# Kernel tuning notes

Measured on AMD Instinct MI355X. Metric: run time of the kernel, lower is better.

## Reference

```python
import jax, jax.numpy as jnp
import numpy as np

N_NODES = 50000
N_EDGES = 800000
IN_F, HID, HEADS, OUT_F = 64, 64, 4, 64
NEG_SLOPE = 0.2


def _gat_conv(x, ei, W, a_src, a_dst, b, H, C):
    """PyG-style GATConv (eval mode, add_self_loops=True, concat=True).
    x: [N, F_in], ei: [2, E], W: [F_in, H*C], a_src/a_dst: [H, C], b: [H*C].
    """
    N = x.shape[0]
    h = (x @ W).reshape(N, H, C)                      # [N,H,C]
    asrc = jnp.einsum('nhc,hc->nh', h, a_src)         # [N,H]
    adst = jnp.einsum('nhc,hc->nh', h, a_dst)         # [N,H]
    src, dst = ei[0], ei[1]
    logits = jax.nn.leaky_relu(asrc[src] + adst[dst], NEG_SLOPE)  # [E,H]
    m = jax.ops.segment_max(logits, dst, num_segments=N)
    m = jnp.where(jnp.isfinite(m), m, 0.0)
    ex = jnp.exp(logits - m[dst])
    denom = jax.ops.segment_sum(ex, dst, num_segments=N)
    alpha = ex / (denom[dst] + 1e-16)                 # [E,H]
    msg = h[src] * alpha[:, :, None]                  # [E,H,C]
    out = jax.ops.segment_sum(msg, dst, num_segments=N)  # [N,H,C]
    return out.reshape(N, H * C) + b


def _add_self_loops(ei, n):
    loops = jnp.arange(n, dtype=ei.dtype)
    return jnp.concatenate([ei, jnp.stack([loops, loops])], axis=1)


def setup_inputs() -> dict:
    key = jax.random.key(0)
    ks = jax.random.split(key, 16)
    x = jax.random.normal(ks[0], (N_NODES, IN_F), dtype=jnp.float32)
    edge_index = jax.random.randint(ks[1], (2, N_EDGES), 0, N_NODES, dtype=jnp.int32)
    s = 0.1
    d = {'x': x, 'edge_index': edge_index}
    # layer 0: IN_F -> HID, HEADS heads
    d['W0'] = jax.random.normal(ks[2], (IN_F, HEADS * HID), jnp.float32) * s
    d['a_src0'] = jax.random.normal(ks[3], (HEADS, HID), jnp.float32) * s
    d['a_dst0'] = jax.random.normal(ks[4], (HEADS, HID), jnp.float32) * s
    d['b0'] = jnp.zeros((HEADS * HID,), jnp.float32)
    # layer 1: HEADS*HID -> HID, HEADS heads
    d['W1'] = jax.random.normal(ks[5], (HEADS * HID, HEADS * HID), jnp.float32) * s
    d['a_src1'] = jax.random.normal(ks[6], (HEADS, HID), jnp.float32) * s
    d['a_dst1'] = jax.random.normal(ks[7], (HEADS, HID), jnp.float32) * s
    d['b1'] = jnp.zeros((HEADS * HID,), jnp.float32)
    # layer 2: HEADS*HID -> OUT_F, 1 head
    d['W2'] = jax.random.normal(ks[8], (HEADS * HID, OUT_F), jnp.float32) * s
    d['a_src2'] = jax.random.normal(ks[9], (1, OUT_F), jnp.float32) * s
    d['a_dst2'] = jax.random.normal(ks[10], (1, OUT_F), jnp.float32) * s
    d['b2'] = jnp.zeros((OUT_F,), jnp.float32)
    return d


def reference(x, edge_index, W0, a_src0, a_dst0, b0, W1, a_src1, a_dst1, b1, W2, a_src2, a_dst2, b2):
    ei = _add_self_loops(edge_index, x.shape[0])
    h = _gat_conv(x, ei, W0, a_src0, a_dst0, b0, HEADS, HID)
    h = jax.nn.elu(h)  # dropout identity in eval
    h = _gat_conv(h, ei, W1, a_src1, a_dst1, b1, HEADS, HID)
    h = jax.nn.elu(h)
    out = _gat_conv(h, ei, W2, a_src2, a_dst2, b2, 1, OUT_F)
    return out
```

## Files before the change

### kernel.cpp

```cpp
#include <hip/hip_runtime.h>
#include <hip/hip_fp16.h>
#include <math.h>

#define NODES 50000
#define EDGES 800000
#define NB_SCAN ((NODES + 1023) / 1024)

typedef __attribute__((ext_vector_type(8))) _Float16 f16x8;
typedef __attribute__((ext_vector_type(4))) _Float16 f16x4;
typedef __attribute__((ext_vector_type(4))) float f32x4;

__device__ __forceinline__ float lrelu02(float x){ return x > 0.f ? x : 0.2f * x; }


__global__ __launch_bounds__(256) void gat_zero(int* __restrict__ p, int n){
  int i = blockIdx.x * 256 + threadIdx.x;
  if (i < n) p[i] = 0;
}

__global__ __launch_bounds__(256) void gat_hist(const int* __restrict__ ei, int* __restrict__ cnt){
  int e = blockIdx.x * 256 + threadIdx.x;
  if (e < EDGES) atomicAdd(&cnt[ei[EDGES + e]], 1);
}

__global__ __launch_bounds__(256) void gat_blocksum(const int* __restrict__ cnt, int* __restrict__ bsums){
  __shared__ int sd[256];
  int t = threadIdx.x, b = blockIdx.x;
  int base = b * 1024 + t * 4, s = 0;
  #pragma unroll
  for (int j = 0; j < 4; j++){ int i = base + j; if (i < NODES) s += cnt[i]; }
  sd[t] = s; __syncthreads();
  for (int o = 128; o > 0; o >>= 1){ if (t < o) sd[t] += sd[t + o]; __syncthreads(); }
  if (t == 0) bsums[b] = sd[0];
}

__global__ void gat_scan_bsums(int* bsums, int nb){
  if (threadIdx.x == 0 && blockIdx.x == 0){
    int run = 0;
    for (int i = 0; i < nb; i++){ int v = bsums[i]; bsums[i] = run; run += v; }
  }
}

__global__ __launch_bounds__(256) void gat_rowptr(int* __restrict__ cnt, const int* __restrict__ bsums,
                                                  int* __restrict__ row_ptr){
  __shared__ int sd[256];
  int t = threadIdx.x, b = blockIdx.x;
  int base = b * 1024 + t * 4;
  int c[4]; int s = 0;
  #pragma unroll
  for (int j = 0; j < 4; j++){
    int i = base + j;
    c[j] = (i < NODES) ? cnt[i] : 0;
    s += c[j];
    if (i < NODES) cnt[i] = 0;
  }
  sd[t] = s; __syncthreads();
  for (int o = 1; o < 256; o <<= 1){
    int v = (t >= o) ? sd[t - o] : 0;
    __syncthreads();
    if (t >= o) sd[t] += v;
    __syncthreads();
  }
  int off = bsums[b] + sd[t] - s;
  #pragma unroll
  for (int j = 0; j < 4; j++){
    int i = base + j;
    if (i < NODES){ row_ptr[i] = off; off += c[j]; }
  }
  if (b == 0 && t == 0) row_ptr[NODES] = EDGES;
}

__global__ __launch_bounds__(256) void gat_scatter(const int* __restrict__ ei, const int* __restrict__ row_ptr,
                                                    int* __restrict__ fill, int* __restrict__ col,
                                                    int* __restrict__ dstarr){
  int e = blockIdx.x * 256 + threadIdx.x;
  if (e < EDGES){
    int s = ei[e], d = ei[EDGES + e];
    int pos = row_ptr[d] + atomicAdd(&fill[d], 1);
    col[pos] = s;
    dstarr[pos] = d;
  }
}


__global__ __launch_bounds__(256) void gat_cvt_h(const float* __restrict__ src, _Float16* __restrict__ dst, int n4){
  int i = blockIdx.x * 256 + threadIdx.x;
  if (i < n4){
    float4 v = *(const float4*)(src + (size_t)i * 4);
    f16x4 h = { (_Float16)v.x, (_Float16)v.y, (_Float16)v.z, (_Float16)v.w };
    *(f16x4*)(dst + (size_t)i * 4) = h;
  }
}

__global__ __launch_bounds__(256) void gat_wt(const float* __restrict__ W, _Float16* __restrict__ Wt, int K, int N){
  int n = blockIdx.x * 256 + threadIdx.x;
  int k = blockIdx.y;
  if (n < N) Wt[(size_t)n * K + k] = (_Float16)W[(size_t)k * N + n];
}

__global__ __launch_bounds__(256) void gat_ws0(const float* __restrict__ W0, const float* __restrict__ a_src0,
                                               const float* __restrict__ a_dst0,
                                               float* __restrict__ ws, float* __restrict__ wd){
  int t = threadIdx.x;
  int h = t >> 6, c = t & 63;
  float s = 0.f, d = 0.f;
  for (int cc = 0; cc < 64; cc++){
    float w = W0[(size_t)c * 256 + h * 64 + cc];
    s += w * a_src0[h * 64 + cc];
    d += w * a_dst0[h * 64 + cc];
  }
  ws[h * 64 + c] = s;
  wd[h * 64 + c] = d;
}


template<int K, int N>
__global__ __launch_bounds__(256) void gat_gemm_mfma(const _Float16* __restrict__ A, const _Float16* __restrict__ Wt,
                                                      _Float16* __restrict__ C, int M){
  constexpr int NT = N / 64;
  constexpr int LDT = 40;
  __shared__ _Float16 As[64][LDT];
  __shared__ _Float16 Bs[N][LDT];

  int tid = threadIdx.x;
  int w = tid >> 6, l = tid & 63;
  int lg = l >> 4, lr = l & 15;
  int bm = blockIdx.x * 64;

  f32x4 acc[4][NT];
  #pragma unroll
  for (int m = 0; m < 4; m++)
    #pragma unroll
    for (int n = 0; n < NT; n++)
      acc[m][n] = (f32x4){0.f, 0.f, 0.f, 0.f};

  int ar = tid >> 2;
  int akc = (tid & 3) * 8;
  bool avalid = (bm + ar) < M;
  const _Float16* aptr = A + (size_t)(bm + ar) * K + akc;

  for (int k0 = 0; k0 < K; k0 += 32){
    float4 av = avalid ? *(const float4*)(aptr + k0) : make_float4(0.f, 0.f, 0.f, 0.f);
    __syncthreads();
    *(float4*)&As[ar][akc] = av;
    #pragma unroll
    for (int c = 0; c < N / 64; c++){
      int idx = c * 256 + tid;
      int n = idx >> 2, kc = (idx & 3) * 8;
      *(float4*)&Bs[n][kc] = *(const float4*)(Wt + (size_t)n * K + k0 + kc);
    }
    __syncthreads();

    f16x8 af[4], bf[NT];
    #pragma unroll
    for (int m = 0; m < 4; m++) af[m] = *(const f16x8*)&As[16 * m + lr][8 * lg];
    #pragma unroll
    for (int n = 0; n < NT; n++) bf[n] = *(const f16x8*)&Bs[w * (N / 4) + 16 * n + lr][8 * lg];
    #pragma unroll
    for (int m = 0; m < 4; m++)
      #pragma unroll
      for (int n = 0; n < NT; n++)
        acc[m][n] = __builtin_amdgcn_mfma_f32_16x16x32_f16(af[m], bf[n], acc[m][n], 0, 0, 0);
  }

  #pragma unroll
  for (int m = 0; m < 4; m++){
    #pragma unroll
    for (int j = 0; j < 4; j++){
      int row = bm + 16 * m + 4 * lg + j;
      if (row < M){
        #pragma unroll
        for (int n = 0; n < NT; n++)
          C[(size_t)row * N + w * (N / 4) + 16 * n + lr] = (_Float16)acc[m][n][j];
      }
    }
  }
}


__global__ __launch_bounds__(256) void gat_gemm_bd(const _Float16* __restrict__ A, const _Float16* __restrict__ Bt,
                                                    const float* __restrict__ bias, _Float16* __restrict__ C, int M){
  int tid = threadIdx.x;
  int w = tid >> 6, l = tid & 63;
  int lg = l >> 4, lr = l & 15;
  int bm = blockIdx.x * 64;

  f32x4 acc[4][4];
  #pragma unroll
  for (int m = 0; m < 4; m++)
    #pragma unroll
    for (int n = 0; n < 4; n++)
      acc[m][n] = (f32x4){0.f, 0.f, 0.f, 0.f};

  f16x8 zf = {};
  #pragma unroll
  for (int ks = 0; ks < 2; ks++){
    int koff = ks * 32;
    f16x8 af[4], bf[4];
    #pragma unroll
    for (int m = 0; m < 4; m++){
      int row = bm + 16 * m + lr;
      af[m] = (row < M) ? *(const f16x8*)(A + (size_t)row * 256 + w * 64 + koff + 8 * lg) : zf;
    }
    #pragma unroll
    for (int n = 0; n < 4; n++)
      bf[n] = *(const f16x8*)(Bt + (size_t)(w * 64 + 16 * n + lr) * 64 + koff + 8 * lg);
    #pragma unroll
    for (int m = 0; m < 4; m++)
      #pragma unroll
      for (int n = 0; n < 4; n++)
        acc[m][n] = __builtin_amdgcn_mfma_f32_16x16x32_f16(af[m], bf[n], acc[m][n], 0, 0, 0);
  }

  #pragma unroll
  for (int m = 0; m < 4; m++){
    #pragma unroll
    for (int j = 0; j < 4; j++){
      int row = bm + 16 * m + 4 * lg + j;
      if (row < M){
        #pragma unroll
        for (int n = 0; n < 4; n++){
          int cc = w * 64 + 16 * n + lr;
          float o = acc[m][n][j] + bias[cc];
          o = o > 0.f ? o : expm1f(o);
          C[(size_t)row * 256 + cc] = (_Float16)o;
        }
      }
    }
  }
}


__global__ __launch_bounds__(256) void gat_attn0(const _Float16* __restrict__ xh, const float* __restrict__ ws,
                                                  const float* __restrict__ wd,
                                                  float* __restrict__ asrc, float* __restrict__ adst, int N){
  int lane = threadIdx.x & 63;
  int wid = threadIdx.x >> 6;
  int n = blockIdx.x * 4 + wid;
  if (n >= N) return;
  float v = (float)xh[(size_t)n * 64 + lane];
  #pragma unroll
  for (int h = 0; h < 4; h++){
    float s1 = v * ws[h * 64 + lane];
    float s2 = v * wd[h * 64 + lane];
    #pragma unroll
    for (int o = 32; o > 0; o >>= 1){ s1 += __shfl_xor(s1, o); s2 += __shfl_xor(s2, o); }
    if (lane == 0){ asrc[n * 4 + h] = s1; adst[n * 4 + h] = s2; }
  }
}

__global__ __launch_bounds__(256) void gat_attn4(const _Float16* __restrict__ h, const float* __restrict__ a_src,
                                                  const float* __restrict__ a_dst,
                                                  float* __restrict__ asrc, float* __restrict__ adst, int N){
  int lane = threadIdx.x & 63;
  int wid = threadIdx.x >> 6;
  int n = blockIdx.x * 4 + wid;
  if (n >= N) return;
  int co = lane * 4;
  f16x4 hv = *(const f16x4*)(h + (size_t)n * 256 + co);
  float4 av = *(const float4*)&a_src[co];
  float4 dv = *(const float4*)&a_dst[co];
  float f0 = (float)hv[0], f1 = (float)hv[1], f2 = (float)hv[2], f3 = (float)hv[3];
  float s1 = f0 * av.x + f1 * av.y + f2 * av.z + f3 * av.w;
  float s2 = f0 * dv.x + f1 * dv.y + f2 * dv.z + f3 * dv.w;
  #pragma unroll
  for (int o = 8; o > 0; o >>= 1){ s1 += __shfl_xor(s1, o); s2 += __shfl_xor(s2, o); }
  if ((lane & 15) == 0){
    int q = lane >> 4;
    asrc[n * 4 + q] = s1;
    adst[n * 4 + q] = s2;
  }
}

__global__ __launch_bounds__(256) void gat_attn1(const _Float16* __restrict__ h, const float* __restrict__ a_src,
                                                  const float* __restrict__ a_dst,
                                                  float* __restrict__ asrc, float* __restrict__ adst, int N){
  int lane = threadIdx.x & 63;
  int wid = threadIdx.x >> 6;
  int n = blockIdx.x * 4 + wid;
  if (n >= N) return;
  float v = (float)h[(size_t)n * 64 + lane];
  float s1 = v * a_src[lane];
  float s2 = v * a_dst[lane];
  #pragma unroll
  for (int o = 32; o > 0; o >>= 1){ s1 += __shfl_xor(s1, o); s2 += __shfl_xor(s2, o); }
  if (lane == 0){ asrc[n] = s1; adst[n] = s2; }
}


__global__ __launch_bounds__(256) void gat_edge_exp0(const int* __restrict__ col, const int* __restrict__ dstarr,
                                                      const float* __restrict__ asrc, const float* __restrict__ adst,
                                                      float* __restrict__ exf){
  int i = blockIdx.x * 256 + threadIdx.x;
  if (i >= EDGES) return;
  int s = col[i], d = dstarr[i];
  float4 a = *(const float4*)&asrc[s * 4];
  float4 b = *(const float4*)&adst[d * 4];
  float4 r;
  r.x = __expf(lrelu02(a.x + b.x));
  r.y = __expf(lrelu02(a.y + b.y));
  r.z = __expf(lrelu02(a.z + b.z));
  r.w = __expf(lrelu02(a.w + b.w));
  *(float4*)&exf[(size_t)i * 4] = r;
}


__global__ __launch_bounds__(256) void gat_aggregate_in64(const _Float16* __restrict__ xh, const float* __restrict__ exf,
                                                           const float* __restrict__ asrc, const float* __restrict__ adst,
                                                           const int* __restrict__ row_ptr, const int* __restrict__ col,
                                                           _Float16* __restrict__ agg){
  int lane = threadIdx.x & 63;
  int wid = threadIdx.x >> 6;
  int d = blockIdx.x * 4 + wid;
  if (d >= NODES) return;

  float4 ad4 = *(const float4*)&adst[d * 4];
  float4 a4  = *(const float4*)&asrc[d * 4];
  float ex0 = __expf(lrelu02(a4.x + ad4.x));
  float ex1 = __expf(lrelu02(a4.y + ad4.y));
  float ex2 = __expf(lrelu02(a4.z + ad4.z));
  float ex3 = __expf(lrelu02(a4.w + ad4.w));
  float xv = (float)xh[(size_t)d * 64 + lane];
  float acc0 = ex0 * xv, acc1 = ex1 * xv, acc2 = ex2 * xv, acc3 = ex3 * xv;
  float den0 = ex0, den1 = ex1, den2 = ex2, den3 = ex3;

  int e0 = row_ptr[d], e1 = row_ptr[d + 1];
  const _Float16* xbase = xh + lane;
  int e = e0;
  for (; e + 4 <= e1; e += 4){
    int s0 = col[e], s1 = col[e + 1], s2 = col[e + 2], s3 = col[e + 3];
    float4 fA = *(const float4*)(exf + (size_t)(e)     * 4);
    float4 fB = *(const float4*)(exf + (size_t)(e + 1) * 4);
    float4 fC = *(const float4*)(exf + (size_t)(e + 2) * 4);
    float4 fD = *(const float4*)(exf + (size_t)(e + 3) * 4);
    float v0 = (float)xbase[(size_t)s0 * 64];
    float v1 = (float)xbase[(size_t)s1 * 64];
    float v2 = (float)xbase[(size_t)s2 * 64];
    float v3 = (float)xbase[(size_t)s3 * 64];
    den0 += fA.x + fB.x + fC.x + fD.x;
    den1 += fA.y + fB.y + fC.y + fD.y;
    den2 += fA.z + fB.z + fC.z + fD.z;
    den3 += fA.w + fB.w + fC.w + fD.w;
    acc0 += fA.x * v0 + fB.x * v1 + fC.x * v2 + fD.x * v3;
    acc1 += fA.y * v0 + fB.y * v1 + fC.y * v2 + fD.y * v3;
    acc2 += fA.z * v0 + fB.z * v1 + fC.z * v2 + fD.z * v3;
    acc3 += fA.w * v0 + fB.w * v1 + fC.w * v2 + fD.w * v3;
  }
  for (; e < e1; e++){
    int s0 = col[e];
    float4 fA = *(const float4*)(exf + (size_t)e * 4);
    float v0 = (float)xbase[(size_t)s0 * 64];
    den0 += fA.x; den1 += fA.y; den2 += fA.z; den3 += fA.w;
    acc0 += fA.x * v0; acc1 += fA.y * v0; acc2 += fA.z * v0; acc3 += fA.w * v0;
  }

  _Float16* ob = agg + (size_t)d * 256 + lane;
  ob[0]   = (_Float16)(acc0 / (den0 + 1e-16f));
  ob[64]  = (_Float16)(acc1 / (den1 + 1e-16f));
  ob[128] = (_Float16)(acc2 / (den2 + 1e-16f));
  ob[192] = (_Float16)(acc3 / (den3 + 1e-16f));
}


template<bool DOELU>
__global__ __launch_bounds__(256) void gat_aggregate4(const _Float16* __restrict__ hH, const float* __restrict__ asrc,
                                                       const float* __restrict__ adst,
                                                       const int* __restrict__ row_ptr, const int* __restrict__ col,
                                                       const float* __restrict__ bias, _Float16* __restrict__ out){
  int lane = threadIdx.x & 63;
  int wid = threadIdx.x >> 6;
  int d = blockIdx.x * 4 + wid;
  if (d >= NODES) return;
  int q = lane >> 4;
  int co = lane * 4;

  float adq = adst[d * 4 + q];

  float ex = __expf(lrelu02(asrc[d * 4 + q] + adq));
  f16x4 hv = *(const f16x4*)(hH + (size_t)d * 256 + co);
  float4 acc = make_float4(ex * (float)hv[0], ex * (float)hv[1], ex * (float)hv[2], ex * (float)hv[3]);
  float den = ex;

  int e0 = row_ptr[d], e1 = row_ptr[d + 1];
  const _Float16* hbase = hH + co;
  int e = e0;
  for (; e + 4 <= e1; e += 4){
    int s0 = col[e], s1 = col[e + 1], s2 = col[e + 2], s3 = col[e + 3];
    float a0 = asrc[s0 * 4 + q], a1 = asrc[s1 * 4 + q], a2 = asrc[s2 * 4 + q], a3 = asrc[s3 * 4 + q];
    f16x4 h0 = *(const f16x4*)(hbase + (size_t)s0 * 256);
    f16x4 h1 = *(const f16x4*)(hbase + (size_t)s1 * 256);
    f16x4 h2 = *(const f16x4*)(hbase + (size_t)s2 * 256);
    f16x4 h3 = *(const f16x4*)(hbase + (size_t)s3 * 256);
    float x0 = __expf(lrelu02(a0 + adq));
    float x1 = __expf(lrelu02(a1 + adq));
    float x2 = __expf(lrelu02(a2 + adq));
    float x3 = __expf(lrelu02(a3 + adq));
    den += x0 + x1 + x2 + x3;
    acc.x += x0 * (float)h0[0] + x1 * (float)h1[0] + x2 * (float)h2[0] + x3 * (float)h3[0];
    acc.y += x0 * (float)h0[1] + x1 * (float)h1[1] + x2 * (float)h2[1] + x3 * (float)h3[1];
    acc.z += x0 * (float)h0[2] + x1 * (float)h1[2] + x2 * (float)h2[2] + x3 * (float)h3[2];
    acc.w += x0 * (float)h0[3] + x1 * (float)h1[3] + x2 * (float)h2[3] + x3 * (float)h3[3];
  }
  for (; e < e1; e++){
    int s0 = col[e];
    float a0 = asrc[s0 * 4 + q];
    f16x4 h0 = *(const f16x4*)(hbase + (size_t)s0 * 256);
    float x0 = __expf(lrelu02(a0 + adq));
    den += x0;
    acc.x += x0 * (float)h0[0]; acc.y += x0 * (float)h0[1];
    acc.z += x0 * (float)h0[2]; acc.w += x0 * (float)h0[3];
  }

  float inv = 1.f / (den + 1e-16f);
  float4 b4 = *(const float4*)&bias[co];
  float4 o = make_float4(acc.x * inv + b4.x, acc.y * inv + b4.y, acc.z * inv + b4.z, acc.w * inv + b4.w);
  if (DOELU){
    o.x = o.x > 0.f ? o.x : expm1f(o.x);
    o.y = o.y > 0.f ? o.y : expm1f(o.y);
    o.z = o.z > 0.f ? o.z : expm1f(o.z);
    o.w = o.w > 0.f ? o.w : expm1f(o.w);
  }
  f16x4 oh = { (_Float16)o.x, (_Float16)o.y, (_Float16)o.z, (_Float16)o.w };
  *(f16x4*)(out + (size_t)d * 256 + co) = oh;
}

__global__ __launch_bounds__(256) void gat_aggregate1(const _Float16* __restrict__ hH, const float* __restrict__ asrc,
                                                       const float* __restrict__ adst,
                                                       const int* __restrict__ row_ptr, const int* __restrict__ col,
                                                       const float* __restrict__ bias, float* __restrict__ out){
  int lane = threadIdx.x & 63;
  int wid = threadIdx.x >> 6;
  int d = blockIdx.x * 4 + wid;
  if (d >= NODES) return;

  float adq = adst[d];
  float ex = __expf(lrelu02(asrc[d] + adq));
  float acc = ex * (float)hH[(size_t)d * 64 + lane];
  float den = ex;

  int e0 = row_ptr[d], e1 = row_ptr[d + 1];
  const _Float16* hbase = hH + lane;
  int e = e0;
  for (; e + 4 <= e1; e += 4){
    int s0 = col[e], s1 = col[e + 1], s2 = col[e + 2], s3 = col[e + 3];
    float a0 = asrc[s0], a1 = asrc[s1], a2 = asrc[s2], a3 = asrc[s3];
    float v0 = (float)hbase[(size_t)s0 * 64];
    float v1 = (float)hbase[(size_t)s1 * 64];
    float v2 = (float)hbase[(size_t)s2 * 64];
    float v3 = (float)hbase[(size_t)s3 * 64];
    float x0 = __expf(lrelu02(a0 + adq));
    float x1 = __expf(lrelu02(a1 + adq));
    float x2 = __expf(lrelu02(a2 + adq));
    float x3 = __expf(lrelu02(a3 + adq));
    den += x0 + x1 + x2 + x3;
    acc += x0 * v0 + x1 * v1 + x2 * v2 + x3 * v3;
  }
  for (; e < e1; e++){
    int s0 = col[e];
    float x0 = __expf(lrelu02(asrc[s0] + adq));
    den += x0;
    acc += x0 * (float)hbase[(size_t)s0 * 64];
  }
  out[(size_t)d * 64 + lane] = acc / (den + 1e-16f) + bias[lane];
}


extern "C" void kernel_launch(void* const* d_in, const int* in_sizes, int n_in,
                              void* d_out, int out_size, void* d_ws, size_t ws_size,
                              hipStream_t stream) {
  const float* x   = (const float*)d_in[0];
  const int*   ei  = (const int*)  d_in[1];
  const float* W0  = (const float*)d_in[2];
  const float* as0 = (const float*)d_in[3];
  const float* ad0 = (const float*)d_in[4];
  const float* b0  = (const float*)d_in[5];
  const float* W1  = (const float*)d_in[6];
  const float* as1 = (const float*)d_in[7];
  const float* ad1 = (const float*)d_in[8];
  const float* b1  = (const float*)d_in[9];
  const float* W2  = (const float*)d_in[10];
  const float* as2 = (const float*)d_in[11];
  const float* ad2 = (const float*)d_in[12];
  const float* b2  = (const float*)d_in[13];
  float* out = (float*)d_out;

  auto al = [](size_t v){ return (v + 255) & ~(size_t)255; };
  char* p = (char*)d_ws;
  int*      row_ptr = (int*)p;      p += al((NODES + 1) * sizeof(int));
  int*      cnt     = (int*)p;      p += al(NODES * sizeof(int));
  int*      bsums   = (int*)p;      p += al(64 * sizeof(int));
  int*      col     = (int*)p;      p += al(EDGES * sizeof(int));
  int*      dstarr  = (int*)p;      p += al(EDGES * sizeof(int));
  float*    exf     = (float*)p;    p += al((size_t)EDGES * 4 * sizeof(float));
  float*    asrc    = (float*)p;    p += al(NODES * 4 * sizeof(float));
  float*    adst    = (float*)p;    p += al(NODES * 4 * sizeof(float));
  _Float16* xh      = (_Float16*)p; p += al((size_t)NODES * 64 * sizeof(_Float16));
  _Float16* hH      = (_Float16*)p; p += al((size_t)NODES * 256 * sizeof(_Float16));
  _Float16* actb    = (_Float16*)p; p += al((size_t)NODES * 256 * sizeof(_Float16));
  _Float16* Wt0     = (_Float16*)p; p += al(256 * 64 * sizeof(_Float16));
  _Float16* Wt1     = (_Float16*)p; p += al(256 * 256 * sizeof(_Float16));
  _Float16* Wt2     = (_Float16*)p; p += al(64 * 256 * sizeof(_Float16));
  float*    ws0     = (float*)p;    p += al(256 * sizeof(float));
  float*    wd0     = (float*)p;    p += al(256 * sizeof(float));

  gat_cvt_h<<<(NODES * 64 / 4 + 255) / 256, 256, 0, stream>>>(x, xh, NODES * 64 / 4);
  gat_wt<<<dim3(1, 64), 256, 0, stream>>>(W0, Wt0, 64, 256);
  gat_wt<<<dim3(1, 256), 256, 0, stream>>>(W1, Wt1, 256, 256);
  gat_wt<<<dim3(1, 256), 256, 0, stream>>>(W2, Wt2, 256, 64);
  gat_ws0<<<1, 256, 0, stream>>>(W0, as0, ad0, ws0, wd0);

  gat_zero<<<(NODES + 255) / 256, 256, 0, stream>>>(cnt, NODES);
  gat_hist<<<(EDGES + 255) / 256, 256, 0, stream>>>(ei, cnt);
  gat_blocksum<<<NB_SCAN, 256, 0, stream>>>(cnt, bsums);
  gat_scan_bsums<<<1, 64, 0, stream>>>(bsums, NB_SCAN);
  gat_rowptr<<<NB_SCAN, 256, 0, stream>>>(cnt, bsums, row_ptr);
  gat_scatter<<<(EDGES + 255) / 256, 256, 0, stream>>>(ei, row_ptr, cnt, col, dstarr);

  const int nodeBlocks = (NODES + 3) / 4;
  const int gemmBlocks = (NODES + 63) / 64;
  const int edgeBlocks = (EDGES + 255) / 256;

  gat_attn0<<<nodeBlocks, 256, 0, stream>>>(xh, ws0, wd0, asrc, adst, NODES);
  gat_edge_exp0<<<edgeBlocks, 256, 0, stream>>>(col, dstarr, asrc, adst, exf);
  gat_aggregate_in64<<<nodeBlocks, 256, 0, stream>>>(xh, exf, asrc, adst, row_ptr, col, hH);
  gat_gemm_bd<<<gemmBlocks, 256, 0, stream>>>(hH, Wt0, b0, actb, NODES);

  gat_gemm_mfma<256, 256><<<gemmBlocks, 256, 0, stream>>>(actb, Wt1, hH, NODES);
  gat_attn4<<<nodeBlocks, 256, 0, stream>>>(hH, as1, ad1, asrc, adst, NODES);
  gat_aggregate4<true><<<nodeBlocks, 256, 0, stream>>>(hH, asrc, adst, row_ptr, col, b1, actb);

  gat_gemm_mfma<256, 64><<<gemmBlocks, 256, 0, stream>>>(actb, Wt2, hH, NODES);
  gat_attn1<<<nodeBlocks, 256, 0, stream>>>(hH, as2, ad2, asrc, adst, NODES);
  gat_aggregate1<<<nodeBlocks, 256, 0, stream>>>(hH, asrc, adst, row_ptr, col, b2, out);
}
```

Before: 377.9 us.

## Precompute head-major edge exps and split layer-1 aggregation per head

For the middle layer, a new edge kernel computes the per-edge exponentials once and stores them head-major. The aggregation kernel then launches one block per head per group of four nodes, so each wavefront handles a single head with 64 channels and reads a contiguous stream of exps instead of recomputing exp from gathered asrc. The gather and aggregation loops in all layers also get an alignment prologue, then load column indices as int4, and the layer-1 and layer-2 loops are unrolled by 8. This trades an extra edge pass and more blocks, each re-reading row_ptr and col per head, for more memory-level parallelism and less exp work inside the aggregation.

```diff
diff --git a/kernel.cpp b/kernel.cpp
--- a/kernel.cpp
+++ b/kernel.cpp
@@ -304,6 +304,20 @@
   *(float4*)&exf[(size_t)i * 4] = r;
 }
 
+__global__ __launch_bounds__(256) void gat_edge_exp4h(const int* __restrict__ col, const int* __restrict__ dstarr,
+                                                       const float* __restrict__ asrc, const float* __restrict__ adst,
+                                                       float* __restrict__ exfh){
+  int i = blockIdx.x * 256 + threadIdx.x;
+  if (i >= EDGES) return;
+  int s = col[i], d = dstarr[i];
+  float4 a = *(const float4*)&asrc[s * 4];
+  float4 b = *(const float4*)&adst[d * 4];
+  exfh[i]             = __expf(lrelu02(a.x + b.x));
+  exfh[EDGES + i]     = __expf(lrelu02(a.y + b.y));
+  exfh[2 * EDGES + i] = __expf(lrelu02(a.z + b.z));
+  exfh[3 * EDGES + i] = __expf(lrelu02(a.w + b.w));
+}
+
 
 __global__ __launch_bounds__(256) void gat_aggregate_in64(const _Float16* __restrict__ xh, const float* __restrict__ exf,
                                                            const float* __restrict__ asrc, const float* __restrict__ adst,
@@ -327,16 +341,23 @@
   int e0 = row_ptr[d], e1 = row_ptr[d + 1];
   const _Float16* xbase = xh + lane;
   int e = e0;
+  for (; e < e1 && (e & 3); e++){
+    int s0 = col[e];
+    float4 fA = *(const float4*)(exf + (size_t)e * 4);
+    float v0 = (float)xbase[(size_t)s0 * 64];
+    den0 += fA.x; den1 += fA.y; den2 += fA.z; den3 += fA.w;
+    acc0 += fA.x * v0; acc1 += fA.y * v0; acc2 += fA.z * v0; acc3 += fA.w * v0;
+  }
   for (; e + 4 <= e1; e += 4){
-    int s0 = col[e], s1 = col[e + 1], s2 = col[e + 2], s3 = col[e + 3];
+    int4 c4 = *(const int4*)&col[e];
     float4 fA = *(const float4*)(exf + (size_t)(e)     * 4);
     float4 fB = *(const float4*)(exf + (size_t)(e + 1) * 4);
     float4 fC = *(const float4*)(exf + (size_t)(e + 2) * 4);
     float4 fD = *(const float4*)(exf + (size_t)(e + 3) * 4);
-    float v0 = (float)xbase[(size_t)s0 * 64];
-    float v1 = (float)xbase[(size_t)s1 * 64];
-    float v2 = (float)xbase[(size_t)s2 * 64];
-    float v3 = (float)xbase[(size_t)s3 * 64];
+    float v0 = (float)xbase[(size_t)c4.x * 64];
+    float v1 = (float)xbase[(size_t)c4.y * 64];
+    float v2 = (float)xbase[(size_t)c4.z * 64];
+    float v3 = (float)xbase[(size_t)c4.w * 64];
     den0 += fA.x + fB.x + fC.x + fD.x;
     den1 += fA.y + fB.y + fC.y + fD.y;
     den2 += fA.z + fB.z + fC.z + fD.z;
@@ -362,67 +383,59 @@
 }
 
 
-template<bool DOELU>
-__global__ __launch_bounds__(256) void gat_aggregate4(const _Float16* __restrict__ hH, const float* __restrict__ asrc,
-                                                       const float* __restrict__ adst,
-                                                       const int* __restrict__ row_ptr, const int* __restrict__ col,
-                                                       const float* __restrict__ bias, _Float16* __restrict__ out){
-  int lane = threadIdx.x & 63;
-  int wid = threadIdx.x >> 6;
-  int d = blockIdx.x * 4 + wid;
-  if (d >= NODES) return;
-  int q = lane >> 4;
-  int co = lane * 4;
+__global__ __launch_bounds__(256) void gat_aggregate4h(const _Float16* __restrict__ hH,
+                                                        const float* __restrict__ exfh,
+                                                        const float* __restrict__ asrc, const float* __restrict__ adst,
+                                                        const int* __restrict__ row_ptr, const int* __restrict__ col,
+                                                        const float* __restrict__ bias, _Float16* __restrict__ out){
+  int bid = blockIdx.x;
+  int r = bid & 7;
+  int q = r >> 1;
+  int dq = (bid >> 3) * 2 + (r & 1);
+  int lane = threadIdx.x & 63, w = threadIdx.x >> 6;
+  int d = dq * 4 + w;
 
   float adq = adst[d * 4 + q];
-
   float ex = __expf(lrelu02(asrc[d * 4 + q] + adq));
-  f16x4 hv = *(const f16x4*)(hH + (size_t)d * 256 + co);
-  float4 acc = make_float4(ex * (float)hv[0], ex * (float)hv[1], ex * (float)hv[2], ex * (float)hv[3]);
   float den = ex;
-
+  const _Float16* hb = hH + q * 64 + lane;
+  float acc = ex * (float)hb[(size_t)d * 256];
+
+  const float* eq = exfh + (size_t)q * EDGES;
   int e0 = row_ptr[d], e1 = row_ptr[d + 1];
-  const _Float16* hbase = hH + co;
   int e = e0;
-  for (; e + 4 <= e1; e += 4){
-    int s0 = col[e], s1 = col[e + 1], s2 = col[e + 2], s3 = col[e + 3];
-    float a0 = asrc[s0 * 4 + q], a1 = asrc[s1 * 4 + q], a2 = asrc[s2 * 4 + q], a3 = asrc[s3 * 4 + q];
-    f16x4 h0 = *(const f16x4*)(hbase + (size_t)s0 * 256);
-    f16x4 h1 = *(const f16x4*)(hbase + (size_t)s1 * 256);
-    f16x4 h2 = *(const f16x4*)(hbase + (size_t)s2 * 256);
-    f16x4 h3 = *(const f16x4*)(hbase + (size_t)s3 * 256);
-    float x0 = __expf(lrelu02(a0 + adq));
-    float x1 = __expf(lrelu02(a1 + adq));
-    float x2 = __expf(lrelu02(a2 + adq));
-    float x3 = __expf(lrelu02(a3 + adq));
-    den += x0 + x1 + x2 + x3;
-    acc.x += x0 * (float)h0[0] + x1 * (float)h1[0] + x2 * (float)h2[0] + x3 * (float)h3[0];
-    acc.y += x0 * (float)h0[1] + x1 * (float)h1[1] + x2 * (float)h2[1] + x3 * (float)h3[1];
-    acc.z += x0 * (float)h0[2] + x1 * (float)h1[2] + x2 * (float)h2[2] + x3 * (float)h3[2];
-    acc.w += x0 * (float)h0[3] + x1 * (float)h1[3] + x2 * (float)h2[3] + x3 * (float)h3[3];
+  for (; e < e1 && (e & 3); e++){
+    float ee = eq[e];
+    den += ee; acc += ee * (float)hb[(size_t)col[e] * 256];
+  }
+  for (; e + 8 <= e1; e += 8){
+    int4 cA = *(const int4*)&col[e];
+    int4 cB = *(const int4*)&col[e + 4];
+    float4 eA = *(const float4*)&eq[e];
+    float4 eB = *(const float4*)&eq[e + 4];
+    float v0 = (float)hb[(size_t)cA.x * 256];
+    float v1 = (float)hb[(size_t)cA.y * 256];
+    float v2 = (float)hb[(size_t)cA.z * 256];
+    float v3 = (float)hb[(size_t)cA.w * 256];
+    float v4 = (float)hb[(size_t)cB.x * 256];
+    float v5 = (float)hb[(size_t)cB.y * 256];
+    float v6 = (float)hb[(size_t)cB.z * 256];
+    float v7 = (float)hb[(size_t)cB.w * 256];
+    den += eA.x + eA.y + eA.z + eA.w + eB.x + eB.y + eB.z + eB.w;
+    acc += eA.x * v0 + eA.y * v1 + eA.z * v2 + eA.w * v3
+         + eB.x * v4 + eB.y * v5 + eB.z * v6 + eB.w * v7;
   }
   for (; e < e1; e++){
-    int s0 = col[e];
-    float a0 = asrc[s0 * 4 + q];
-    f16x4 h0 = *(const f16x4*)(hbase + (size_t)s0 * 256);
-    float x0 = __expf(lrelu02(a0 + adq));
-    den += x0;
-    acc.x += x0 * (float)h0[0]; acc.y += x0 * (float)h0[1];
-    acc.z += x0 * (float)h0[2]; acc.w += x0 * (float)h0[3];
-  }
-
-  float inv = 1.f / (den + 1e-16f);
-  float4 b4 = *(const float4*)&bias[co];
-  float4 o = make_float4(acc.x * inv + b4.x, acc.y * inv + b4.y, acc.z * inv + b4.z, acc.w * inv + b4.w);
-  if (DOELU){
-    o.x = o.x > 0.f ? o.x : expm1f(o.x);
-    o.y = o.y > 0.f ? o.y : expm1f(o.y);
-    o.z = o.z > 0.f ? o.z : expm1f(o.z);
-    o.w = o.w > 0.f ? o.w : expm1f(o.w);
-  }
-  f16x4 oh = { (_Float16)o.x, (_Float16)o.y, (_Float16)o.z, (_Float16)o.w };
-  *(f16x4*)(out + (size_t)d * 256 + co) = oh;
-}
+    float ee = eq[e];
+    den += ee; acc += ee * (float)hb[(size_t)col[e] * 256];
+  }
+
+  int cc = q * 64 + lane;
+  float o = acc / (den + 1e-16f) + bias[cc];
+  o = o > 0.f ? o : expm1f(o);
+  out[(size_t)d * 256 + cc] = (_Float16)o;
+}
+
 
 __global__ __launch_bounds__(256) void gat_aggregate1(const _Float16* __restrict__ hH, const float* __restrict__ asrc,
                                                        const float* __restrict__ adst,
@@ -441,19 +454,31 @@
   int e0 = row_ptr[d], e1 = row_ptr[d + 1];
   const _Float16* hbase = hH + lane;
   int e = e0;
-  for (; e + 4 <= e1; e += 4){
-    int s0 = col[e], s1 = col[e + 1], s2 = col[e + 2], s3 = col[e + 3];
-    float a0 = asrc[s0], a1 = asrc[s1], a2 = asrc[s2], a3 = asrc[s3];
-    float v0 = (float)hbase[(size_t)s0 * 64];
-    float v1 = (float)hbase[(size_t)s1 * 64];
-    float v2 = (float)hbase[(size_t)s2 * 64];
-    float v3 = (float)hbase[(size_t)s3 * 64];
-    float x0 = __expf(lrelu02(a0 + adq));
-    float x1 = __expf(lrelu02(a1 + adq));
-    float x2 = __expf(lrelu02(a2 + adq));
-    float x3 = __expf(lrelu02(a3 + adq));
-    den += x0 + x1 + x2 + x3;
-    acc += x0 * v0 + x1 * v1 + x2 * v2 + x3 * v3;
+  for (; e < e1 && (e & 3); e++){
+    int s0 = col[e];
+    float x0 = __expf(lrelu02(asrc[s0] + adq));
+    den += x0;
+    acc += x0 * (float)hbase[(size_t)s0 * 64];
+  }
+  for (; e + 8 <= e1; e += 8){
+    int4 cA = *(const int4*)&col[e];
+    int4 cB = *(const int4*)&col[e + 4];
+    float a0 = asrc[cA.x], a1 = asrc[cA.y], a2 = asrc[cA.z], a3 = asrc[cA.w];
+    float a4 = asrc[cB.x], a5 = asrc[cB.y], a6 = asrc[cB.z], a7 = asrc[cB.w];
+    float v0 = (float)hbase[(size_t)cA.x * 64];
+    float v1 = (float)hbase[(size_t)cA.y * 64];
+    float v2 = (float)hbase[(size_t)cA.z * 64];
+    float v3 = (float)hbase[(size_t)cA.w * 64];
+    float v4 = (float)hbase[(size_t)cB.x * 64];
+    float v5 = (float)hbase[(size_t)cB.y * 64];
+    float v6 = (float)hbase[(size_t)cB.z * 64];
+    float v7 = (float)hbase[(size_t)cB.w * 64];
+    float x0 = __expf(lrelu02(a0 + adq)), x1 = __expf(lrelu02(a1 + adq));
+    float x2 = __expf(lrelu02(a2 + adq)), x3 = __expf(lrelu02(a3 + adq));
+    float x4 = __expf(lrelu02(a4 + adq)), x5 = __expf(lrelu02(a5 + adq));
+    float x6 = __expf(lrelu02(a6 + adq)), x7 = __expf(lrelu02(a7 + adq));
+    den += x0 + x1 + x2 + x3 + x4 + x5 + x6 + x7;
+    acc += x0 * v0 + x1 * v1 + x2 * v2 + x3 * v3 + x4 * v4 + x5 * v5 + x6 * v6 + x7 * v7;
   }
   for (; e < e1; e++){
     int s0 = col[e];
@@ -527,7 +552,8 @@
 
   gat_gemm_mfma<256, 256><<<gemmBlocks, 256, 0, stream>>>(actb, Wt1, hH, NODES);
   gat_attn4<<<nodeBlocks, 256, 0, stream>>>(hH, as1, ad1, asrc, adst, NODES);
-  gat_aggregate4<true><<<nodeBlocks, 256, 0, stream>>>(hH, asrc, adst, row_ptr, col, b1, actb);
+  gat_edge_exp4h<<<edgeBlocks, 256, 0, stream>>>(col, dstarr, asrc, adst, exf);
+  gat_aggregate4h<<<NODES, 256, 0, stream>>>(hH, exf, asrc, adst, row_ptr, col, b1, actb);
 
   gat_gemm_mfma<256, 64><<<gemmBlocks, 256, 0, stream>>>(actb, Wt2, hH, NODES);
   gat_attn1<<<nodeBlocks, 256, 0, stream>>>(hH, as2, ad2, asrc, adst, NODES);
```

Measured after the change: 478.8 us. 26.7% more time.
